# Kernel tuning notes

Hardware: AMD Instinct MI355X
Metric: run time of the kernel (lower is better)

The kernel has to match this reference:

```python
import jax, jax.numpy as jnp
import numpy as np

HEADS = 8
DIM_HEAD = 128
SCALE = DIM_HEAD ** -0.5
EPS = 1e-5


def layer_norm(t, w, b):
    mu = t.mean(-1, keepdims=True)
    var = ((t - mu) ** 2).mean(-1, keepdims=True)
    return (t - mu) * jax.lax.rsqrt(var + EPS) * w + b


def setup_inputs() -> dict:
    key = jax.random.key(0)
    ks = jax.random.split(key, 8)
    b, n, dim = 4, 1024, 1024
    inner = HEADS * DIM_HEAD  # 1024
    w = 0.02
    return {
        "x": jax.random.normal(ks[0], (b, n, dim), jnp.float32),
        "cond_info": jax.random.normal(ks[1], (b, n, dim), jnp.float32),
        "ref": jax.random.normal(ks[2], (b, n, dim), jnp.float32),
        "ln_w": jnp.ones((dim,), jnp.float32),
        "ln_b": jnp.zeros((dim,), jnp.float32),
        "cln_w": jnp.ones((dim,), jnp.float32),
        "cln_b": jnp.zeros((dim,), jnp.float32),
        "Wk": jax.random.normal(ks[3], (3 * dim, inner), jnp.float32) * w,
        "Wv": jax.random.normal(ks[4], (2 * dim, inner), jnp.float32) * w,
        "Wo": jax.random.normal(ks[5], (inner, dim), jnp.float32) * w,
        "bo": jnp.zeros((dim,), jnp.float32),
        "th_w": jax.random.normal(ks[6], (HEADS, HEADS), jnp.float32) * 0.3,
        "cth_w": jax.random.normal(ks[7], (HEADS, HEADS), jnp.float32) * 0.3,
    }


def reference(x, cond_info, ref, ln_w, ln_b, cln_w, cln_b, Wk, Wv, Wo, bo, th_w, cth_w):
    b, n, _ = x.shape
    h, d = HEADS, DIM_HEAD
    xn = layer_norm(x, ln_w, ln_b)
    rn = layer_norm(ref, ln_w, ln_b)
    cn = layer_norm(cond_info, cln_w, cln_b)
    # projections (y_to_q output is unused in the original forward; omitted)
    cond = jnp.concatenate([xn, cn, rn], axis=-1) @ Wk   # [b, n, h*d]
    refv = jnp.concatenate([xn, rn], axis=-1) @ Wv       # [b, n, h*d]
    split = lambda t: t.reshape(b, n, h, d).transpose(0, 2, 1, 3)  # b h n d
    cond, refv = split(cond), split(refv)
    sim = jnp.einsum('bhid,bhjd->bhij', cond, refv) * SCALE
    attn = jax.nn.softmax(sim, axis=-1)           # row softmax
    context_attn = jax.nn.softmax(sim, axis=-2)   # column softmax
    # talking heads: 1x1 conv over head dim, weight [out_h, in_h]
    attn = jnp.einsum('gh,bhij->bgij', th_w, attn)
    context_attn = jnp.einsum('gh,bhij->bgij', cth_w, context_attn)
    out = jnp.einsum('bhij,bhjd->bhid', attn, refv)
    context_out = jnp.einsum('bhji,bhjd->bhid', context_attn, cond)
    merge = lambda t: t.transpose(0, 2, 1, 3).reshape(b, n, h * d)
    out = merge(out) @ Wo + bo
    context_out = merge(context_out)
    return out, context_out
```

## Files before the change

### kernel.cpp

```cpp
#include <hip/hip_runtime.h>
#include <hip/hip_bf16.h>
#include <stdint.h>

typedef unsigned short u16;
typedef __attribute__((ext_vector_type(8))) short bf16x8;
typedef __attribute__((ext_vector_type(4))) float f32x4;

#define HEADS 8
#define DHEAD 128
#define NSEQ 1024
#define BATCH 4
#define DIM 1024
#define ATT_SCALE 0.088388347648318447f

static __device__ __forceinline__ float bf2f(u16 u){
  union { unsigned int i; float f; } c; c.i = ((unsigned int)u) << 16; return c.f;
}
static __device__ __forceinline__ u16 f2bf(float f){
  union { float f; unsigned int i; } c; c.f = f;
  unsigned int x = c.i;
  return (u16)((x + 0x7fffu + ((x >> 16) & 1u)) >> 16);
}

static __device__ __forceinline__ void gload_lds16(const void* g, void* l){
  __builtin_amdgcn_global_load_lds((__attribute__((address_space(1))) void*)(g),
                                   (__attribute__((address_space(3))) void*)(l),
                                   16, 0, 0);
}

__global__ __launch_bounds__(256)
void ln3_kernel(const float* __restrict__ x, const float* __restrict__ ref,
                const float* __restrict__ cinfo,
                const float* __restrict__ ln_w, const float* __restrict__ ln_b,
                const float* __restrict__ cln_w, const float* __restrict__ cln_b,
                u16* __restrict__ xn, u16* __restrict__ rn, u16* __restrict__ cn)
{
  const int z = blockIdx.y;
  const float* src = (z==0) ? x : (z==1) ? ref : cinfo;
  const float* w   = (z==2) ? cln_w : ln_w;
  const float* b   = (z==2) ? cln_b : ln_b;
  u16* out         = (z==0) ? xn : (z==1) ? rn : cn;

  const int row = blockIdx.x;
  const int t = threadIdx.x;
  const float* xr = src + (size_t)row * DIM;
  float4 v4 = *(const float4*)(xr + t*4);
  float v[4] = {v4.x, v4.y, v4.z, v4.w};
  float s = v[0]+v[1]+v[2]+v[3];
  __shared__ float red[256];
  red[t] = s; __syncthreads();
  for (int o=128;o;o>>=1){ if (t<o) red[t]+=red[t+o]; __syncthreads(); }
  const float mean = red[0] * (1.0f/DIM);
  __syncthreads();
  s = 0.f;
#pragma unroll
  for (int i=0;i<4;i++){ float d = v[i]-mean; s += d*d; }
  red[t] = s; __syncthreads();
  for (int o=128;o;o>>=1){ if (t<o) red[t]+=red[t+o]; __syncthreads(); }
  const float rstd = rsqrtf(red[0]*(1.0f/DIM) + 1e-5f);
  float4 w4 = *(const float4*)(w + t*4);
  float4 b4 = *(const float4*)(b + t*4);
  float wv[4] = {w4.x, w4.y, w4.z, w4.w};
  float bv[4] = {b4.x, b4.y, b4.z, b4.w};
  union { uint2 u; u16 s[4]; } ov;
#pragma unroll
  for (int i=0;i<4;i++)
    ov.s[i] = f2bf((v[i]-mean)*rstd*wv[i] + bv[i]);
  *(uint2*)(out + (size_t)row*DIM + t*4) = ov.u;
}

__global__ __launch_bounds__(256)
void wcvt_kernel(const float* __restrict__ Wk, const float* __restrict__ Wv,
                 const float* __restrict__ Wo,
                 u16* __restrict__ WkT, u16* __restrict__ WvT, u16* __restrict__ WoT)
{
  const int z = blockIdx.z;
  const int K = (z==0) ? 3072 : (z==1) ? 2048 : 1024;
  if ((int)blockIdx.x*32 >= K) return;
  const float* W = (z==0) ? Wk : (z==1) ? Wv : Wo;
  u16* WT = (z==0) ? WkT : (z==1) ? WvT : WoT;
  __shared__ float tile[32][33];
  const int k0 = blockIdx.x*32, n0 = blockIdx.y*32;
  const int t = threadIdx.x, tc = t&31, tr = t>>5;
#pragma unroll
  for (int p=0;p<4;p++)
    tile[tr+p*8][tc] = W[(size_t)(k0+tr+p*8)*DIM + n0+tc];
  __syncthreads();
#pragma unroll
  for (int p=0;p<4;p++)
    WT[(size_t)(n0+tr+p*8)*K + k0+tc] = f2bf(tile[tc][tr+p*8]);
}

template<int BK>
__global__ __launch_bounds__(256)
void gemm_kernel(const u16* __restrict__ A0, const u16* __restrict__ A1,
                 const u16* __restrict__ A2, const u16* __restrict__ A0b,
                 const u16* __restrict__ A1b,
                 const u16* __restrict__ B1, const u16* __restrict__ B2,
                 void* __restrict__ Cv, void* __restrict__ Cv2,
                 const float* __restrict__ bias,
                 int K1, int K2, int lda, int ldb1, int ldb2, int ldc,
                 long a_plane, long b_plane, long c_plane,
                 int epi1, int epi2, int z_split, float alpha)
{
  constexpr int SUBS = BK/32;
  __shared__ __attribute__((aligned(16))) u16 sA[2][SUBS*4096];
  __shared__ __attribute__((aligned(16))) u16 sB[2][SUBS*4096];
  const int t = threadIdx.x;
  const int m0 = blockIdx.y*128, n0 = blockIdx.x*128;
  const int zz = blockIdx.z;
  const bool side = (zz >= z_split);
  const int z = side ? (zz - z_split) : zz;
  const u16* a0 = (side ? A0b : A0) + (size_t)z*a_plane;
  const u16* a1 = (side ? A1b : A1) + (size_t)z*a_plane;
  const u16* a2 = A2 + (size_t)z*a_plane;
  const u16* bB = (side ? B2 : B1) + (size_t)z*b_plane;
  void* Cp = side ? Cv2 : Cv;
  const int EPI = side ? epi2 : epi1;
  const int K   = side ? K2 : K1;
  const int ldb = side ? ldb2 : ldb1;

  const int wave = t>>6, lane = t&63;
  const int wm = (wave>>1)*64, wn = (wave&1)*64;
  const int lm = lane&15, q = lane>>4;

  const f32x4 zero4 = {0.f,0.f,0.f,0.f};
  f32x4 acc[4][4];
#pragma unroll
  for (int i=0;i<4;i++)
#pragma unroll
    for (int j=0;j<4;j++) acc[i][j] = zero4;

  const int arowblk = wave*32;

  const int KT = K / BK;

  auto issueA = [&](int kt, int buf){
    const int kg = kt*BK, seg = kg>>10, ka = kg&1023;
    const u16* Ap = (seg==0) ? a0 : (seg==1 ? a1 : a2);
#pragma unroll
    for (int sub=0; sub<SUBS; ++sub)
#pragma unroll
      for (int rr=0; rr<2; ++rr){
        const int rb = arowblk + rr*16;
        gload_lds16(Ap + (size_t)(m0+rb+lm)*lda + (ka + sub*32 + q*8),
                    &sA[buf][sub*4096 + rb*32]);
      }
  };
  auto issueB = [&](int kt, int buf){
    const int kg = kt*BK;
#pragma unroll
    for (int sub=0; sub<SUBS; ++sub)
#pragma unroll
      for (int rr=0; rr<2; ++rr){
        const int rb = arowblk + rr*16;
        gload_lds16(bB + (size_t)(n0+rb+lm)*ldb + (kg + sub*32 + q*8),
                    &sB[buf][sub*4096 + rb*32]);
      }
  };

  issueA(0, 0);
  issueB(0, 0);

  int cur = 0;
  for (int kt=0; kt<KT; ++kt){
    __syncthreads();
    if (kt+1 < KT){
      issueA(kt+1, cur^1);
      issueB(kt+1, cur^1);
    }
#pragma unroll
    for (int sub=0; sub<SUBS; ++sub){
      bf16x8 af[4], bfr[4];
#pragma unroll
      for (int f=0; f<4; ++f){
        af[f]  = *(const bf16x8*)&sA[cur][sub*4096 + ((wm>>4)+f)*512 + lane*8];
        bfr[f] = *(const bf16x8*)&sB[cur][sub*4096 + ((wn>>4)+f)*512 + lane*8];
      }
#pragma unroll
      for (int fm=0; fm<4; ++fm)
#pragma unroll
        for (int fn=0; fn<4; ++fn)
          acc[fm][fn] = __builtin_amdgcn_mfma_f32_16x16x32_bf16(af[fm], bfr[fn], acc[fm][fn], 0, 0, 0);
    }
    cur ^= 1;
  }

#pragma unroll
  for (int fm=0; fm<4; ++fm){
#pragma unroll
    for (int fn=0; fn<4; ++fn){
#pragma unroll
      for (int r=0; r<4; ++r){
        const int m = m0 + wm + fm*16 + q*4 + r;
        const int n = n0 + wn + fn*16 + lm;
        float val = acc[fm][fn][r] * alpha;
        if (EPI == 0){
          ((u16*)Cp)[(size_t)z*c_plane + (size_t)m*ldc + n] = f2bf(val);
        } else if (EPI == 1){
          ((u16*)Cp)[((size_t)(z>>3)*NSEQ + m)*DIM + (size_t)(z&7)*DHEAD + n] = f2bf(val);
        } else if (EPI == 2){
          ((float*)Cp)[(size_t)m*ldc + n] = val + bias[n];
        } else if (EPI == 3){
          ((u16*)Cp)[(size_t)(((m>>10)*HEADS + (n>>7))*NSEQ + (m&1023))*DHEAD + (n&127)] = f2bf(val);
        } else {
          ((float*)Cp)[((size_t)(z>>3)*NSEQ + m)*DIM + (size_t)(z&7)*DHEAD + n] = val;
        }
      }
    }
  }
}

__global__ __launch_bounds__(256)
void gemm8_kernel(const u16* __restrict__ A, const u16* __restrict__ B,
                  float* __restrict__ P)
{
  __shared__ __attribute__((aligned(16))) u16 sA[2][4096];
  __shared__ __attribute__((aligned(16))) u16 sB[2][4096];
  const int t = threadIdx.x;
  const int bid = blockIdx.x;
  const int w = (bid & 7)*128 + (bid >> 3);
  const int x = w & 7;
  const int y = (w >> 3) & 31;
  const int s = w >> 8;
  const int m0 = y*128, n0 = x*128, k0 = s*256;

  const int wave = t>>6, lane = t&63;
  const int wm = (wave>>1)*64, wn = (wave&1)*64;
  const int lm = lane&15, q = lane>>4;

  const f32x4 zero4 = {0.f,0.f,0.f,0.f};
  f32x4 acc[4][4];
#pragma unroll
  for (int i=0;i<4;i++)
#pragma unroll
    for (int j=0;j<4;j++) acc[i][j] = zero4;

  const int arowblk = wave*32;

  auto issueA = [&](int kt, int buf){
    const int kg = k0 + (kt<<5);
#pragma unroll
    for (int rr=0; rr<2; ++rr){
      const int rb = arowblk + rr*16;
      gload_lds16(A + (size_t)(m0+rb+lm)*1024 + (kg + q*8), &sA[buf][rb*32]);
    }
  };
  auto issueB = [&](int kt, int buf){
    const int kg = k0 + (kt<<5);
#pragma unroll
    for (int rr=0; rr<2; ++rr){
      const int rb = arowblk + rr*16;
      gload_lds16(B + (size_t)(n0+rb+lm)*1024 + (kg + q*8), &sB[buf][rb*32]);
    }
  };

  issueA(0, 0); issueB(0, 0);

  int cur = 0;
  for (int kt=0; kt<8; ++kt){
    __syncthreads();
    if (kt+1 < 8){
      issueA(kt+1, cur^1);
      issueB(kt+1, cur^1);
    }
    bf16x8 af[4], bfr[4];
#pragma unroll
    for (int f=0; f<4; ++f){
      af[f]  = *(const bf16x8*)&sA[cur][((wm>>4)+f)*512 + lane*8];
      bfr[f] = *(const bf16x8*)&sB[cur][((wn>>4)+f)*512 + lane*8];
    }
#pragma unroll
    for (int fm=0; fm<4; ++fm)
#pragma unroll
      for (int fn=0; fn<4; ++fn)
        acc[fm][fn] = __builtin_amdgcn_mfma_f32_16x16x32_bf16(af[fm], bfr[fn], acc[fm][fn], 0, 0, 0);
    cur ^= 1;
  }

  float* Pp = P + (size_t)s*4194304;
#pragma unroll
  for (int fm=0; fm<4; ++fm){
#pragma unroll
    for (int fn=0; fn<4; ++fn){
#pragma unroll
      for (int r=0; r<4; ++r){
        const int m = m0 + wm + fm*16 + q*4 + r;
        const int n = n0 + wn + fn*16 + lm;
        Pp[(size_t)m*1024 + n] = acc[fm][fn][r];
      }
    }
  }
}

__global__ __launch_bounds__(256)
void red8_kernel(const float* __restrict__ P, const float* __restrict__ bias,
                 float* __restrict__ out)
{
  const int idx = blockIdx.x*256 + threadIdx.x;
  const float4* P4 = (const float4*)P;
  float4 a = P4[idx];
  float4 b = P4[idx + 1048576];
  float4 c = P4[idx + 2097152];
  float4 d = P4[idx + 3145728];
  float4 bb = ((const float4*)bias)[idx & 255];
  float4 o;
  o.x = a.x + b.x + c.x + d.x + bb.x;
  o.y = a.y + b.y + c.y + d.y + bb.y;
  o.z = a.z + b.z + c.z + d.z + bb.z;
  o.w = a.w + b.w + c.w + d.w + bb.w;
  ((float4*)out)[idx] = o;
}

__global__ __launch_bounds__(256)
void transpose2_kernel(const u16* __restrict__ cond, const u16* __restrict__ refv,
                       u16* __restrict__ condT, u16* __restrict__ refvT)
{
  __shared__ u16 tile[32][33];
  const int zz = blockIdx.z;
  const u16* X = (zz < 32) ? cond : refv;
  u16* XT      = (zz < 32) ? condT : refvT;
  const int z = zz & 31;
  const int i0 = blockIdx.y*32, d0 = blockIdx.x*32;
  const int t = threadIdx.x;
  const int tc = t & 31, tr = t >> 5;
  const u16* Xp = X + (size_t)z*NSEQ*DHEAD;
#pragma unroll
  for (int p=0;p<4;p++){
    int i = tr + p*8;
    tile[i][tc] = Xp[(size_t)(i0+i)*DHEAD + d0 + tc];
  }
  __syncthreads();
  u16* Op = XT + (size_t)z*DHEAD*NSEQ;
#pragma unroll
  for (int p=0;p<4;p++){
    int d = tr + p*8;
    Op[(size_t)(d0+d)*NSEQ + i0 + tc] = tile[tc][d];
  }
}

__global__ __launch_bounds__(256)
void stats_kernel(const u16* __restrict__ sim,
                  float* __restrict__ rmax, float* __restrict__ rrcp,
                  float* __restrict__ cmax, float* __restrict__ crcp)
{
  __shared__ float smx[4][64], ssm[4][64];
  if (blockIdx.x < 8192){
    const int wave = threadIdx.x >> 6, lane = threadIdx.x & 63;
    const int row = blockIdx.x*4 + wave;
    const u16* sr = sim + (size_t)row * NSEQ;
    float v[16]; float m = -1e30f;
#pragma unroll
    for (int c=0;c<16;c++){ v[c] = bf2f(sr[lane + c*64]); m = fmaxf(m, v[c]); }
#pragma unroll
    for (int off=32; off; off>>=1) m = fmaxf(m, __shfl_xor(m, off));
    float s = 0.f;
#pragma unroll
    for (int c=0;c<16;c++) s += __expf(v[c]-m);
#pragma unroll
    for (int off=32; off; off>>=1) s += __shfl_xor(s, off);
    if (lane == 0){ rmax[row] = m; rrcp[row] = 1.0f/s; }
  } else {
    const int t = threadIdx.x;
    const int jl = t & 63, slice = t >> 6;
    const int c = (blockIdx.x - 8192)*64 + jl;
    const int bh = c >> 10, j = c & 1023;
    const u16* sp = sim + (size_t)bh*NSEQ*NSEQ + j + (size_t)(slice*256)*NSEQ;
    float m0=-1e30f, m1=-1e30f, m2=-1e30f, m3=-1e30f;
    for (int i=0;i<256;i+=4){
      m0 = fmaxf(m0, bf2f(sp[(size_t)(i  )*NSEQ]));
      m1 = fmaxf(m1, bf2f(sp[(size_t)(i+1)*NSEQ]));
      m2 = fmaxf(m2, bf2f(sp[(size_t)(i+2)*NSEQ]));
      m3 = fmaxf(m3, bf2f(sp[(size_t)(i+3)*NSEQ]));
    }
    smx[slice][jl] = fmaxf(fmaxf(m0,m1), fmaxf(m2,m3));
    __syncthreads();
    const float M = fmaxf(fmaxf(smx[0][jl], smx[1][jl]),
                          fmaxf(smx[2][jl], smx[3][jl]));
    float s0=0.f, s1=0.f, s2=0.f, s3=0.f;
    for (int i=0;i<256;i+=4){
      s0 += __expf(bf2f(sp[(size_t)(i  )*NSEQ]) - M);
      s1 += __expf(bf2f(sp[(size_t)(i+1)*NSEQ]) - M);
      s2 += __expf(bf2f(sp[(size_t)(i+2)*NSEQ]) - M);
      s3 += __expf(bf2f(sp[(size_t)(i+3)*NSEQ]) - M);
    }
    ssm[slice][jl] = s0+s1+s2+s3;
    __syncthreads();
    if (slice == 0){
      float S = ssm[0][jl] + ssm[1][jl] + ssm[2][jl] + ssm[3][jl];
      cmax[c] = M; crcp[c] = 1.0f/S;
    }
  }
}

__global__ __launch_bounds__(256)
void mix_kernel(u16* simam,
                const float* __restrict__ rmax, const float* __restrict__ rrcp,
                const float* __restrict__ cmax, const float* __restrict__ crcp,
                const float* __restrict__ thw, const float* __restrict__ cthw,
                u16* __restrict__ cmT)
{
  __shared__ float s_th[64], s_cth[64];
  __shared__ u16 s_cm[8][32][33];
  const int t = threadIdx.x;
  if (t < 64){ s_th[t] = thw[t]; s_cth[t] = cthw[t]; }
  __syncthreads();
  const int b = blockIdx.z, i0 = blockIdx.y*32, j0 = blockIdx.x*32;
  const int tj = t & 31, ti = t >> 5;
  for (int p=0;p<4;p++){
    const int i = ti + p*8;
    float a[8], c[8];
#pragma unroll
    for (int h=0;h<8;h++){
      const int bh = b*8 + h;
      const float v = bf2f(simam[((size_t)bh*NSEQ + (i0+i))*NSEQ + j0 + tj]);
      a[h] = __expf(v - rmax[(size_t)bh*NSEQ + i0+i]) * rrcp[(size_t)bh*NSEQ + i0+i];
      c[h] = __expf(v - cmax[(size_t)bh*NSEQ + j0+tj]) * crcp[(size_t)bh*NSEQ + j0+tj];
    }
#pragma unroll
    for (int g=0;g<8;g++){
      float sa = 0.f, sc = 0.f;
#pragma unroll
      for (int h=0;h<8;h++){ sa += s_th[g*8+h]*a[h]; sc += s_cth[g*8+h]*c[h]; }
      simam[((size_t)(b*8+g)*NSEQ + (i0+i))*NSEQ + j0 + tj] = f2bf(sa);
      s_cm[g][i][tj] = f2bf(sc);
    }
  }
  __syncthreads();
#pragma unroll
  for (int g=0;g<8;g++){
#pragma unroll
    for (int p=0;p<4;p++){
      const int j = ti + p*8;
      cmT[((size_t)(b*8+g)*NSEQ + (j0+j))*NSEQ + i0 + tj] = s_cm[g][tj][j];
    }
  }
}

extern "C" void kernel_launch(void* const* d_in, const int* in_sizes, int n_in,
                              void* d_out, int out_size, void* d_ws, size_t ws_size,
                              hipStream_t stream)
{
  const float* x     = (const float*)d_in[0];
  const float* cinfo = (const float*)d_in[1];
  const float* ref   = (const float*)d_in[2];
  const float* ln_w  = (const float*)d_in[3];
  const float* ln_b  = (const float*)d_in[4];
  const float* cln_w = (const float*)d_in[5];
  const float* cln_b = (const float*)d_in[6];
  const float* Wk    = (const float*)d_in[7];
  const float* Wv    = (const float*)d_in[8];
  const float* Wo    = (const float*)d_in[9];
  const float* bo    = (const float*)d_in[10];
  const float* thw   = (const float*)d_in[11];
  const float* cthw  = (const float*)d_in[12];
  float* out = (float*)d_out;

  char* ws = (char*)d_ws;
  u16* xn    = (u16*)(ws + 0);
  u16* cn    = (u16*)(ws + 8388608);
  u16* rn    = (u16*)(ws + 16777216);
  u16* cond  = (u16*)(ws + 25165824);
  u16* refv  = (u16*)(ws + 33554432);
  u16* condT = (u16*)(ws + 41943040);
  u16* refvT = (u16*)(ws + 50331648);
  u16* sim   = (u16*)(ws + 58720256);
  u16* cmT   = (u16*)(ws + 125829120);
  u16* WkT   = (u16*)(ws + 192937984);
  u16* WvT   = (u16*)(ws + 199229440);
  u16* WoT   = (u16*)(ws + 203423744);
  float* rmax = (float*)(ws + 8388608);
  float* rrcp = (float*)(ws + 8388608 + 131072);
  float* cmax = (float*)(ws + 8388608 + 262144);
  float* crcp = (float*)(ws + 8388608 + 393216);
  u16* out_pre = (u16*)(ws + 0);

  ln3_kernel<<<dim3(4096,3), 256, 0, stream>>>(x, ref, cinfo, ln_w, ln_b,
                                               cln_w, cln_b, xn, rn, cn);

  wcvt_kernel<<<dim3(96,32,3), 256, 0, stream>>>(Wk, Wv, Wo, WkT, WvT, WoT);

  gemm_kernel<64><<<dim3(8,32,2), 256, 0, stream>>>(
      xn, cn, rn, xn, rn, WkT, WvT, cond, refv, nullptr,
      3072, 2048, DIM, 3072, 2048, 0, 0, 0, 0, 3, 3, 1, 1.0f);

  transpose2_kernel<<<dim3(4,32,64), 256, 0, stream>>>(cond, refv, condT, refvT);

  gemm_kernel<32><<<dim3(8,8,32), 256, 0, stream>>>(
      cond, cond, cond, cond, cond, refv, refv, sim, sim, nullptr,
      DHEAD, DHEAD, DHEAD, DHEAD, DHEAD, NSEQ,
      (long)NSEQ*DHEAD, (long)NSEQ*DHEAD, (long)NSEQ*NSEQ, 0, 0, 1000000, ATT_SCALE);

  stats_kernel<<<8704, 256, 0, stream>>>(sim, rmax, rrcp, cmax, crcp);

  mix_kernel<<<dim3(32,32,4), 256, 0, stream>>>(sim, rmax, rrcp, cmax, crcp, thw, cthw, cmT);

  gemm_kernel<64><<<dim3(1,8,64), 256, 0, stream>>>(
      sim, sim, sim, cmT, cmT, refvT, condT, out_pre, out + (size_t)BATCH*NSEQ*DIM, nullptr,
      1024, 1024, NSEQ, NSEQ, NSEQ, 0,
      (long)NSEQ*NSEQ, (long)DHEAD*NSEQ, 0, 1, 4, 32, 1.0f);

  gemm8_kernel<<<1024, 256, 0, stream>>>(out_pre, WoT, (float*)sim);
  red8_kernel<<<4096, 256, 0, stream>>>((const float*)sim, bo, out);
}
```

Before: 467.9 us.

## Add single-wave 64x64 GEMM kernel with swizzled grid for projection and PV GEMMs

Adds a new GEMM kernel that runs one 64-thread wave per block. Each block computes a 64x64 tile with double-buffered direct global-to-LDS loads and 16x16x32 bf16 MFMAs, and no block-level barriers. A 1D grid is remapped with an XCD-style swizzle. The kernel replaces the 256-thread tiled GEMM for the QKV-style projection and for the attention-value GEMMs, aiming to raise parallelism and drop the synchronisation overhead. The trade-off is smaller tiles with less operand reuse per block, and scalar per-element epilogue stores.

Result: slower. 594.1 us (+27.0%).

```diff
diff --git a/kernel.cpp b/kernel.cpp
--- a/kernel.cpp
+++ b/kernel.cpp
@@ -89,6 +89,116 @@
 #pragma unroll
   for (int p=0;p<4;p++)
     WT[(size_t)(n0+tr+p*8)*K + k0+tc] = f2bf(tile[tc][tr+p*8]);
+}
+
+__global__ __launch_bounds__(64)
+void gemm1w_kernel(const u16* __restrict__ A0, const u16* __restrict__ A1,
+                   const u16* __restrict__ A2, const u16* __restrict__ A0b,
+                   const u16* __restrict__ A1b,
+                   const u16* __restrict__ B1, const u16* __restrict__ B2,
+                   void* __restrict__ Cv, void* __restrict__ Cv2,
+                   const float* __restrict__ bias,
+                   int K1, int K2, int lda, int ldb1, int ldb2, int ldc,
+                   long a_plane, long b_plane, long c_plane,
+                   int epi1, int epi2, int z_split, int NXT, int NYT,
+                   float alpha)
+{
+  __shared__ __attribute__((aligned(16))) u16 sA[2][2048];
+  __shared__ __attribute__((aligned(16))) u16 sB[2][2048];
+  const int lane = threadIdx.x;
+  const int nb = gridDim.x;
+  const int bid = blockIdx.x;
+  const int swz = (bid & 7)*(nb >> 3) + (bid >> 3);
+  const int per_z = NXT*NYT;
+  const int zz = swz / per_z;
+  const int rr_ = swz - zz*per_z;
+  const int x  = rr_ / NYT;
+  const int y  = rr_ - x*NYT;
+  const int m0 = y*64, n0 = x*64;
+  const bool side = (zz >= z_split);
+  const int z = side ? (zz - z_split) : zz;
+  const u16* a0 = (side ? A0b : A0) + (size_t)z*a_plane;
+  const u16* a1 = (side ? A1b : A1) + (size_t)z*a_plane;
+  const u16* a2 = A2 + (size_t)z*a_plane;
+  const u16* bB = (side ? B2 : B1) + (size_t)z*b_plane;
+  void* Cp = side ? Cv2 : Cv;
+  const int EPI = side ? epi2 : epi1;
+  const int K   = side ? K2 : K1;
+  const int ldb = side ? ldb2 : ldb1;
+
+  const int lm = lane&15, q = lane>>4;
+
+  const f32x4 zero4 = {0.f,0.f,0.f,0.f};
+  f32x4 acc[4][4];
+#pragma unroll
+  for (int i=0;i<4;i++)
+#pragma unroll
+    for (int j=0;j<4;j++) acc[i][j] = zero4;
+
+  auto issueA = [&](int kt, int buf){
+    const int kg = kt<<5, seg = kg>>10, ka = kg&1023;
+    const u16* Ap = (seg==0) ? a0 : (seg==1 ? a1 : a2);
+#pragma unroll
+    for (int rr=0; rr<4; ++rr)
+      gload_lds16(Ap + (size_t)(m0+rr*16+lm)*lda + (ka + q*8), &sA[buf][rr*512]);
+  };
+  auto issueB = [&](int kt, int buf){
+    const int kg = kt<<5;
+#pragma unroll
+    for (int rr=0; rr<4; ++rr)
+      gload_lds16(bB + (size_t)(n0+rr*16+lm)*ldb + (kg + q*8), &sB[buf][rr*512]);
+  };
+
+  const int KT = K >> 5;
+  issueA(0, 0);
+  issueB(0, 0);
+
+  int cur = 0;
+  for (int kt=0; kt<KT; ++kt){
+    if (kt+1 < KT){
+      issueA(kt+1, cur^1);
+      issueB(kt+1, cur^1);
+      asm volatile("s_waitcnt vmcnt(8)" ::: "memory");
+    } else {
+      asm volatile("s_waitcnt vmcnt(0)" ::: "memory");
+    }
+    bf16x8 af[4], bfr[4];
+#pragma unroll
+    for (int f=0; f<4; ++f){
+      af[f]  = *(const bf16x8*)&sA[cur][f*512 + lane*8];
+      bfr[f] = *(const bf16x8*)&sB[cur][f*512 + lane*8];
+    }
+#pragma unroll
+    for (int fm=0; fm<4; ++fm)
+#pragma unroll
+      for (int fn=0; fn<4; ++fn)
+        acc[fm][fn] = __builtin_amdgcn_mfma_f32_16x16x32_bf16(af[fm], bfr[fn], acc[fm][fn], 0, 0, 0);
+    cur ^= 1;
+  }
+
+#pragma unroll
+  for (int fm=0; fm<4; ++fm){
+#pragma unroll
+    for (int fn=0; fn<4; ++fn){
+#pragma unroll
+      for (int r=0; r<4; ++r){
+        const int m = m0 + fm*16 + q*4 + r;
+        const int n = n0 + fn*16 + lm;
+        float val = acc[fm][fn][r] * alpha;
+        if (EPI == 0){
+          ((u16*)Cp)[(size_t)z*c_plane + (size_t)m*ldc + n] = f2bf(val);
+        } else if (EPI == 1){
+          ((u16*)Cp)[((size_t)(z>>3)*NSEQ + m)*DIM + (size_t)(z&7)*DHEAD + n] = f2bf(val);
+        } else if (EPI == 2){
+          ((float*)Cp)[(size_t)m*ldc + n] = val + bias[n];
+        } else if (EPI == 3){
+          ((u16*)Cp)[(size_t)(((m>>10)*HEADS + (n>>7))*NSEQ + (m&1023))*DHEAD + (n&127)] = f2bf(val);
+        } else {
+          ((float*)Cp)[((size_t)(z>>3)*NSEQ + m)*DIM + (size_t)(z&7)*DHEAD + n] = val;
+        }
+      }
+    }
+  }
 }
 
 template<int BK>
@@ -480,9 +590,9 @@
 
   wcvt_kernel<<<dim3(96,32,3), 256, 0, stream>>>(Wk, Wv, Wo, WkT, WvT, WoT);
 
-  gemm_kernel<64><<<dim3(8,32,2), 256, 0, stream>>>(
+  gemm1w_kernel<<<2048, 64, 0, stream>>>(
       xn, cn, rn, xn, rn, WkT, WvT, cond, refv, nullptr,
-      3072, 2048, DIM, 3072, 2048, 0, 0, 0, 0, 3, 3, 1, 1.0f);
+      3072, 2048, DIM, 3072, 2048, 0, 0, 0, 0, 3, 3, 1, 16, 64, 1.0f);
 
   transpose2_kernel<<<dim3(4,32,64), 256, 0, stream>>>(cond, refv, condT, refvT);
 
@@ -495,10 +605,10 @@
 
   mix_kernel<<<dim3(32,32,4), 256, 0, stream>>>(sim, rmax, rrcp, cmax, crcp, thw, cthw, cmT);
 
-  gemm_kernel<64><<<dim3(1,8,64), 256, 0, stream>>>(
+  gemm1w_kernel<<<2048, 64, 0, stream>>>(
       sim, sim, sim, cmT, cmT, refvT, condT, out_pre, out + (size_t)BATCH*NSEQ*DIM, nullptr,
       1024, 1024, NSEQ, NSEQ, NSEQ, 0,
-      (long)NSEQ*NSEQ, (long)DHEAD*NSEQ, 0, 1, 4, 32, 1.0f);
+      (long)NSEQ*NSEQ, (long)DHEAD*NSEQ, 0, 1, 4, 32, 2, 16, 1.0f);
 
   gemm8_kernel<<<1024, 256, 0, stream>>>(out_pre, WoT, (float*)sim);
   red8_kernel<<<4096, 256, 0, stream>>>((const float*)sim, bo, out);
```

## Split-K the fused QKV projection GEMM into per-segment partials plus reduction

Applied to the files above, without the earlier changes.

Replaces the single projection GEMM (512 tiles with K=3072/2048) by a split-K kernel that computes each concatenated input segment (xn, cn, rn) as a separate K=1024 tile, giving 1280 blocks with a grid swizzle. Partial fp32 results go to scratch buffers reused from the sim/cmT workspace. A second kernel sums them, converts to bf16 and writes them in head-split layout. The goal is more parallelism and better CU occupancy, at the cost of roughly 80MB of extra fp32 partial traffic and an extra launch.

Result: slower. 524.9 us (+12.2%).

```diff
diff --git a/kernel.cpp b/kernel.cpp
--- a/kernel.cpp
+++ b/kernel.cpp
@@ -89,6 +89,121 @@
 #pragma unroll
   for (int p=0;p<4;p++)
     WT[(size_t)(n0+tr+p*8)*K + k0+tc] = f2bf(tile[tc][tr+p*8]);
+}
+
+__global__ __launch_bounds__(256)
+void gemmsk2_kernel(const u16* __restrict__ xn, const u16* __restrict__ cn,
+                    const u16* __restrict__ rn,
+                    const u16* __restrict__ WkT, const u16* __restrict__ WvT,
+                    float* __restrict__ Pc, float* __restrict__ Pr)
+{
+  __shared__ __attribute__((aligned(16))) u16 sA[2][4096];
+  __shared__ __attribute__((aligned(16))) u16 sB[2][4096];
+  const int t = threadIdx.x;
+  const int bid = blockIdx.x;
+  const int swz = (bid & 7)*160 + (bid >> 3);
+  const bool condside = swz < 768;
+  const int w = condside ? swz : swz - 768;
+  const int s = w >> 8;
+  const int rem = w & 255;
+  const int x = rem & 7, y = rem >> 3;
+  const int m0 = y*128, n0 = x*128;
+  const u16* A = condside ? (s==0 ? xn : (s==1 ? cn : rn))
+                          : (s==0 ? xn : rn);
+  const u16* B = (condside ? WkT : WvT) + s*1024;
+  const int ldb = condside ? 3072 : 2048;
+  float* P = (condside ? Pc : Pr) + (size_t)s*4194304;
+
+  const int wave = t>>6, lane = t&63;
+  const int wm = (wave>>1)*64, wn = (wave&1)*64;
+  const int lm = lane&15, q = lane>>4;
+
+  const f32x4 zero4 = {0.f,0.f,0.f,0.f};
+  f32x4 acc[4][4];
+#pragma unroll
+  for (int i=0;i<4;i++)
+#pragma unroll
+    for (int j=0;j<4;j++) acc[i][j] = zero4;
+
+  const int arowblk = wave*32;
+
+  auto issueA = [&](int kt, int buf){
+    const int kg = kt<<5;
+#pragma unroll
+    for (int rr=0; rr<2; ++rr){
+      const int rb = arowblk + rr*16;
+      gload_lds16(A + (size_t)(m0+rb+lm)*1024 + (kg + q*8), &sA[buf][rb*32]);
+    }
+  };
+  auto issueB = [&](int kt, int buf){
+    const int kg = kt<<5;
+#pragma unroll
+    for (int rr=0; rr<2; ++rr){
+      const int rb = arowblk + rr*16;
+      gload_lds16(B + (size_t)(n0+rb+lm)*ldb + (kg + q*8), &sB[buf][rb*32]);
+    }
+  };
+
+  issueA(0, 0); issueB(0, 0);
+
+  int cur = 0;
+  for (int kt=0; kt<32; ++kt){
+    __syncthreads();
+    if (kt+1 < 32){
+      issueA(kt+1, cur^1);
+      issueB(kt+1, cur^1);
+    }
+    bf16x8 af[4], bfr[4];
+#pragma unroll
+    for (int f=0; f<4; ++f){
+      af[f]  = *(const bf16x8*)&sA[cur][((wm>>4)+f)*512 + lane*8];
+      bfr[f] = *(const bf16x8*)&sB[cur][((wn>>4)+f)*512 + lane*8];
+    }
+#pragma unroll
+    for (int fm=0; fm<4; ++fm)
+#pragma unroll
+      for (int fn=0; fn<4; ++fn)
+        acc[fm][fn] = __builtin_amdgcn_mfma_f32_16x16x32_bf16(af[fm], bfr[fn], acc[fm][fn], 0, 0, 0);
+    cur ^= 1;
+  }
+
+#pragma unroll
+  for (int fm=0; fm<4; ++fm){
+#pragma unroll
+    for (int fn=0; fn<4; ++fn){
+#pragma unroll
+      for (int r=0; r<4; ++r){
+        const int m = m0 + wm + fm*16 + q*4 + r;
+        const int n = n0 + wn + fn*16 + lm;
+        P[(size_t)m*1024 + n] = acc[fm][fn][r];
+      }
+    }
+  }
+}
+
+__global__ __launch_bounds__(256)
+void redsk2_kernel(const float* __restrict__ Pc, const float* __restrict__ Pr,
+                   u16* __restrict__ cond, u16* __restrict__ refv)
+{
+  const int bid = blockIdx.x;
+  const bool condside = bid < 4096;
+  const int idx = (condside ? bid : bid-4096)*256 + threadIdx.x;
+  const float4* P4 = (const float4*)(condside ? Pc : Pr);
+  float4 a = P4[idx];
+  float4 b = P4[idx + 1048576];
+  float4 o;
+  o.x = a.x + b.x; o.y = a.y + b.y; o.z = a.z + b.z; o.w = a.w + b.w;
+  if (condside){
+    float4 c = P4[idx + 2097152];
+    o.x += c.x; o.y += c.y; o.z += c.z; o.w += c.w;
+  }
+  const int nlin = idx*4;
+  const int m = nlin >> 10, n = nlin & 1023;
+  u16* dst = condside ? cond : refv;
+  union { uint2 u; u16 s[4]; } ov;
+  ov.s[0] = f2bf(o.x); ov.s[1] = f2bf(o.y);
+  ov.s[2] = f2bf(o.z); ov.s[3] = f2bf(o.w);
+  *(uint2*)&dst[((size_t)((m>>10)*HEADS + (n>>7))*NSEQ + (m&1023))*DHEAD + (n&127)] = ov.u;
 }
 
 template<int BK>
@@ -480,9 +595,10 @@
 
   wcvt_kernel<<<dim3(96,32,3), 256, 0, stream>>>(Wk, Wv, Wo, WkT, WvT, WoT);
 
-  gemm_kernel<64><<<dim3(8,32,2), 256, 0, stream>>>(
-      xn, cn, rn, xn, rn, WkT, WvT, cond, refv, nullptr,
-      3072, 2048, DIM, 3072, 2048, 0, 0, 0, 0, 3, 3, 1, 1.0f);
+  gemmsk2_kernel<<<1280, 256, 0, stream>>>(xn, cn, rn, WkT, WvT,
+                                           (float*)sim, (float*)cmT);
+  redsk2_kernel<<<8192, 256, 0, stream>>>((const float*)sim, (const float*)cmT,
+                                          cond, refv);
 
   transpose2_kernel<<<dim3(4,32,64), 256, 0, stream>>>(cond, refv, condT, refvT);
 
```
